# Kernel optimization log

Hardware: AMD Instinct MI355X
Metric: run time of the kernel (lower is better)

## Reference

```python
import jax, jax.numpy as jnp
import numpy as np

N_SRC = 100000
N_DST = 100000
E = 500000
D = 128
L = 2


def _sage(x_src, x_dst, e_src, e_dst, W_self, W_neigh, b):
    # DGL SAGEConv('mean'): out = x_dst @ W_self^T + mean_neighbors(x_src) @ W_neigh^T + b
    n_dst = x_dst.shape[0]
    msg_sum = jax.ops.segment_sum(x_src[e_src], e_dst, num_segments=n_dst)  # [n_dst, D]
    deg = jax.ops.segment_sum(jnp.ones((e_dst.shape[0],), x_src.dtype), e_dst, num_segments=n_dst)
    h_neigh = msg_sum / jnp.maximum(deg, 1.0)[:, None]  # isolated nodes -> 0
    return x_dst @ W_self.T + h_neigh @ W_neigh.T + b


def setup_inputs() -> dict:
    key = jax.random.key(0)
    ks = jax.random.split(key, 10)
    s = 1.0 / np.sqrt(D)
    return {
        "x_src": jax.random.normal(ks[0], (N_SRC, D), jnp.float32),
        "x_dst": jax.random.normal(ks[1], (N_DST, D), jnp.float32),
        "e_src": jax.random.randint(ks[2], (E,), 0, N_SRC, jnp.int32),
        "e_dst": jax.random.randint(ks[3], (E,), 0, N_DST, jnp.int32),
        "W_ship_self": jax.random.normal(ks[4], (L, D, D), jnp.float32) * s,
        "W_ship_neigh": jax.random.normal(ks[5], (L, D, D), jnp.float32) * s,
        "b_ship": jnp.zeros((L, D), jnp.float32),
        "W_rev_self": jax.random.normal(ks[6], (L, D, D), jnp.float32) * s,
        "W_rev_neigh": jax.random.normal(ks[7], (L, D, D), jnp.float32) * s,
        "b_rev": jnp.zeros((L, D), jnp.float32),
    }


def reference(x_src, x_dst, e_src, e_dst, W_ship_self, W_ship_neigh, b_ship,
              W_rev_self, W_rev_neigh, b_rev):
    h_s, h_d = x_src, x_dst
    n_layers = W_ship_self.shape[0]
    for l in range(n_layers):
        # ('source','ship','destination'): messages source -> destination
        new_d = _sage(h_s, h_d, e_src, e_dst, W_ship_self[l], W_ship_neigh[l], b_ship[l])
        # ('destination','rev_ship','source'): messages destination -> source
        new_s = _sage(h_d, h_s, e_dst, e_src, W_rev_self[l], W_rev_neigh[l], b_rev[l])
        h_d = jax.nn.relu(new_d)
        h_s = jax.nn.relu(new_s)
        # dropout p=0.0 (eval) -> identity
    return h_s, h_d
```

## Files before the change

### kernel.cpp

```cpp
#include <hip/hip_runtime.h>
#include <hip/hip_bf16.h>

#define NN 100000
#define EDGES 500000
#define DD 128
#define NBKT 196
#define SLACK 3584
#define CHUNK 4096
#define BPD ((EDGES + CHUNK - 1) / CHUNK)

typedef short bf16x8 __attribute__((ext_vector_type(8)));
typedef float f32x4  __attribute__((ext_vector_type(4)));
typedef float f32x2  __attribute__((ext_vector_type(2)));

__device__ __forceinline__ unsigned short f2bf(float f) {
    unsigned u = __float_as_uint(f);
    u += 0x7fffu + ((u >> 16) & 1u);
    return (unsigned short)(u >> 16);
}

__global__ void f2bx_kernel(const float* __restrict__ a, const float* __restrict__ b,
                            unsigned short* __restrict__ oa, unsigned short* __restrict__ ob) {
    const float* in = blockIdx.y ? b : a;
    unsigned short* out = blockIdx.y ? ob : oa;
    int i = blockIdx.x * 256 + threadIdx.x;
    float4 v = ((const float4*)in)[i];
    ushort4 o;
    o.x = f2bf(v.x); o.y = f2bf(v.y); o.z = f2bf(v.z); o.w = f2bf(v.w);
    ((ushort4*)out)[i] = o;
}

__global__ void f2bw_kernel(const float* __restrict__ w0, const float* __restrict__ w1,
                            const float* __restrict__ w2, const float* __restrict__ w3,
                            unsigned short* __restrict__ o0, unsigned short* __restrict__ o1,
                            unsigned short* __restrict__ o2, unsigned short* __restrict__ o3) {
    const float* in; unsigned short* out;
    switch (blockIdx.y) {
        case 0: in = w0; out = o0; break;
        case 1: in = w1; out = o1; break;
        case 2: in = w2; out = o2; break;
        default: in = w3; out = o3; break;
    }
    int i = blockIdx.x * 256 + threadIdx.x;
    float4 v = ((const float4*)in)[i];
    ushort4 o;
    o.x = f2bf(v.x); o.y = f2bf(v.y); o.z = f2bf(v.z); o.w = f2bf(v.w);
    ((ushort4*)out)[i] = o;
}

__global__ __launch_bounds__(256) void bin_scatter_kernel(
    const int* __restrict__ e_src, const int* __restrict__ e_dst,
    int* __restrict__ gcnt,
    unsigned* __restrict__ recbin)
{
    const int dir = blockIdx.y;
    const int t = threadIdx.x;
    const int c0 = blockIdx.x * CHUNK;
    const int nvalid = min(CHUNK, EDGES - c0);
    const int* __restrict__ TGT = dir ? e_src : e_dst;
    const int* __restrict__ PAY = dir ? e_dst : e_src;

    __shared__ int hist[256];
    __shared__ int lbase[256];
    __shared__ int lofs[256];
    __shared__ int scanA[256], scanB[256];
    __shared__ int laddr[CHUNK];
    __shared__ unsigned lrec[CHUNK];

    hist[t] = 0;
    __syncthreads();

    int myb[16], myslot[16];
    unsigned myrec[16];
    #pragma unroll
    for (int j = 0; j < 16; ++j) {
        int e = c0 + j * 256 + t;
        myb[j] = -1;
        if (e < EDGES) {
            int tgt = TGT[e], pay = PAY[e];
            int b = tgt >> 9;
            myb[j] = b;
            myrec[j] = ((unsigned)pay << 9) | (unsigned)(tgt & 511);
            myslot[j] = atomicAdd(&hist[b], 1);
        }
    }
    __syncthreads();
    int cnt = hist[t];
    lbase[t] = (cnt > 0) ? atomicAdd(&gcnt[dir * 256 + t], cnt) : 0;
    scanA[t] = cnt;
    __syncthreads();
    int* pa = scanA; int* pb = scanB;
    for (int d = 1; d < 256; d <<= 1) {
        pb[t] = pa[t] + (t >= d ? pa[t - d] : 0);
        __syncthreads();
        int* tmp = pa; pa = pb; pb = tmp;
    }
    lofs[t] = pa[t] - cnt;
    __syncthreads();
    #pragma unroll
    for (int j = 0; j < 16; ++j) {
        if (myb[j] >= 0) {
            int b = myb[j];
            int pos = lofs[b] + myslot[j];
            int g = lbase[b] + myslot[j];
            lrec[pos] = myrec[j];
            laddr[pos] = (g < SLACK) ? (b * SLACK + g) : -1;
        }
    }
    __syncthreads();
    unsigned* __restrict__ out = recbin + (size_t)dir * NBKT * SLACK;
    #pragma unroll
    for (int j = 0; j < 16; ++j) {
        int i = j * 256 + t;
        if (i < nvalid) {
            int a = laddr[i];
            if (a >= 0) out[a] = lrec[i];
        }
    }
}

__global__ void bucket_scan_kernel(const int* __restrict__ gcnt, int* __restrict__ csr_base) {
    int t = threadIdx.x;
    __shared__ int A[256], B[256];
    for (int dir = 0; dir < 2; ++dir) {
        int c = (t < NBKT) ? min(gcnt[dir * 256 + t], SLACK) : 0;
        A[t] = c;
        __syncthreads();
        int* pa = A; int* pb = B;
        for (int d = 1; d < 256; d <<= 1) {
            pb[t] = pa[t] + (t >= d ? pa[t - d] : 0);
            __syncthreads();
            int* tmp = pa; pa = pb; pb = tmp;
        }
        if (t < NBKT) csr_base[dir * 200 + t] = pa[t] - c;
        if (t == 0)   csr_base[dir * 200 + NBKT] = pa[255];
        __syncthreads();
    }
}

__global__ __launch_bounds__(256) void fine_place_kernel(
    const unsigned* __restrict__ recbin, const int* __restrict__ gcnt,
    const int* __restrict__ csr_base,
    int* __restrict__ rp_dst, int* __restrict__ rp_src,
    float* __restrict__ inv_dst, float* __restrict__ inv_src,
    int* __restrict__ csr_dst, int* __restrict__ csr_src)
{
    const int dir = blockIdx.y;
    const int bkt = blockIdx.x;
    const int t = threadIdx.x;
    int*   __restrict__ rp  = dir ? rp_src  : rp_dst;
    float* __restrict__ inv = dir ? inv_src : inv_dst;
    int*   __restrict__ csr = dir ? csr_src : csr_dst;
    const unsigned* __restrict__ recs = recbin + ((size_t)dir * NBKT + bkt) * SLACK;
    const int cnt = min(gcnt[dir * 256 + bkt], SLACK);
    const int cbase = csr_base[dir * 200 + bkt];
    const int n0 = bkt * 512;

    __shared__ int deg[512];
    __shared__ int sA[512], sB[512];
    __shared__ int cur[512];
    deg[t] = 0; deg[t + 256] = 0;
    __syncthreads();
    for (int i = t; i < cnt; i += 256)
        atomicAdd(&deg[recs[i] & 511u], 1);
    __syncthreads();
    sA[t] = deg[t]; sA[t + 256] = deg[t + 256];
    __syncthreads();
    int* pa = sA; int* pb = sB;
    for (int d = 1; d < 512; d <<= 1) {
        pb[t]       = pa[t]       + (t >= d           ? pa[t - d]       : 0);
        pb[t + 256] = pa[t + 256] + ((t + 256) >= d   ? pa[t + 256 - d] : 0);
        __syncthreads();
        int* tmp = pa; pa = pb; pb = tmp;
    }
    #pragma unroll
    for (int k = 0; k < 2; ++k) {
        int i = t + k * 256;
        int off = pa[i] - deg[i];
        cur[i] = off;
        int node = n0 + i;
        if (node < NN) {
            rp[node] = cbase + off;
            inv[node] = 1.0f / (float)max(deg[i], 1);
        }
    }
    if (bkt == NBKT - 1 && t == 0) rp[NN] = csr_base[dir * 200 + NBKT];
    __syncthreads();
    for (int i = t; i < cnt; i += 256) {
        unsigned r = recs[i];
        int p = atomicAdd(&cur[r & 511u], 1);
        csr[cbase + p] = (int)(r >> 9);
    }
}

__global__ __launch_bounds__(256) void aggregate3_kernel(
    const unsigned short* __restrict__ h0, const int* __restrict__ rp0,
    const int* __restrict__ csr0, unsigned short* __restrict__ ag0,
    const unsigned short* __restrict__ h1, const int* __restrict__ rp1,
    const int* __restrict__ csr1, unsigned short* __restrict__ ag1)
{
    const int dir = blockIdx.y;
    const unsigned short* __restrict__ h = dir ? h1 : h0;
    const int* __restrict__ rp   = dir ? rp1 : rp0;
    const int* __restrict__ csr  = dir ? csr1 : csr0;
    unsigned short* __restrict__ agg = dir ? ag1 : ag0;

    const int t  = blockIdx.x * 256 + threadIdx.x;
    const int g  = t >> 4;
    const int sl = t & 15;

    const int beg = rp[g], end = rp[g + 1];
    const unsigned short* __restrict__ hp = h + sl * 8;

    f32x2 acc[4];
    #pragma unroll
    for (int k = 0; k < 4; ++k) acc[k] = (f32x2){0.f, 0.f};

    int cidx[8];
    #pragma unroll
    for (int j = 0; j < 8; ++j)
        cidx[j] = (beg + j < end) ? csr[beg + j] : -1;

    bf16x8 v[8];
    #pragma unroll
    for (int j = 0; j < 8; ++j)
        if (cidx[j] >= 0)
            v[j] = *(const bf16x8*)(hp + (size_t)cidx[j] * DD);

    #pragma unroll
    for (int j = 0; j < 8; ++j) {
        if (cidx[j] >= 0) {
            const unsigned* pu = (const unsigned*)&v[j];
            #pragma unroll
            for (int k = 0; k < 4; ++k) {
                unsigned u = pu[k];
                acc[k] += (f32x2){__uint_as_float(u << 16),
                                  __uint_as_float(u & 0xffff0000u)};
            }
        }
    }

    for (int i = beg + 8; i < end; ++i) {
        int c = csr[i];
        bf16x8 w = *(const bf16x8*)(hp + (size_t)c * DD);
        const unsigned* pu = (const unsigned*)&w;
        #pragma unroll
        for (int k = 0; k < 4; ++k) {
            unsigned u = pu[k];
            acc[k] += (f32x2){__uint_as_float(u << 16),
                              __uint_as_float(u & 0xffff0000u)};
        }
    }

    const float sc = 1.0f / (float)max(end - beg, 1);
    uint4 ov;
    ov.x = (unsigned)f2bf(acc[0].x * sc) | ((unsigned)f2bf(acc[0].y * sc) << 16);
    ov.y = (unsigned)f2bf(acc[1].x * sc) | ((unsigned)f2bf(acc[1].y * sc) << 16);
    ov.z = (unsigned)f2bf(acc[2].x * sc) | ((unsigned)f2bf(acc[2].y * sc) << 16);
    ov.w = (unsigned)f2bf(acc[3].x * sc) | ((unsigned)f2bf(acc[3].y * sc) << 16);
    *(uint4*)(agg + (size_t)g * DD + sl * 8) = ov;
}

__global__ __launch_bounds__(512, 4) void mfma_gemm6_kernel(
    const unsigned short* __restrict__ Hs0, const unsigned short* __restrict__ Ha0,
    const unsigned short* __restrict__ Ws0, const unsigned short* __restrict__ Wn0,
    const float* __restrict__ bias0, float* __restrict__ outF0, unsigned short* __restrict__ outB0,
    const unsigned short* __restrict__ Hs1, const unsigned short* __restrict__ Ha1,
    const unsigned short* __restrict__ Ws1, const unsigned short* __restrict__ Wn1,
    const float* __restrict__ bias1, float* __restrict__ outF1, unsigned short* __restrict__ outB1,
    int M)
{
    const int dir = blockIdx.y;
    const unsigned short* __restrict__ Hself = dir ? Hs1 : Hs0;
    const unsigned short* __restrict__ Hagg  = dir ? Ha1 : Ha0;
    const unsigned short* __restrict__ Wself = dir ? Ws1 : Ws0;
    const unsigned short* __restrict__ Wneigh= dir ? Wn1 : Wn0;
    const float* __restrict__ bias = dir ? bias1 : bias0;
    float* __restrict__ outF = dir ? outF1 : outF0;
    unsigned short* __restrict__ outB = dir ? outB1 : outB0;

    __shared__ __align__(16) unsigned short sW[128 * 256];
    const int tid  = threadIdx.x;
    const int lane = tid & 63;
    const int w    = tid >> 6;
    const int row0 = blockIdx.x * 512;

    #pragma unroll
    for (int i = 0; i < 8; ++i) {
        int q = i * 512 + tid;
        int n = q >> 5, c = q & 31;
        const unsigned short* src = (c < 16) ? (Wself + n * 128 + c * 8)
                                             : (Wneigh + n * 128 + (c - 16) * 8);
        int d = n * 256 + (c & 24) * 8 + (((c ^ n) & 7) * 8);
        *(uint4*)(sW + d) = *(const uint4*)src;
    }

    const int mbase = (w >> 1) * 64;
    const int nbase = (w & 1) * 64;
    const int l15 = lane & 15;
    const int l4  = lane >> 4;

    __syncthreads();

    #pragma unroll
    for (int h = 0; h < 2; ++h) {
        const int r0 = row0 + h * 256;

        int voff[4];
        #pragma unroll
        for (int mt = 0; mt < 4; ++mt) {
            int grow = r0 + mbase + mt * 16 + l15;
            if (grow >= M) grow = M - 1;
            voff[mt] = grow * 128 + l4 * 8;
        }

        f32x4 acc[4][4];
        #pragma unroll
        for (int mt = 0; mt < 4; ++mt)
            #pragma unroll
            for (int nt = 0; nt < 4; ++nt) acc[mt][nt] = (f32x4){0.f, 0.f, 0.f, 0.f};

        bf16x8 a_cur[4], a_nxt[4];
        #pragma unroll
        for (int mt = 0; mt < 4; ++mt) a_cur[mt] = *(const bf16x8*)(Hself + voff[mt]);

        #pragma unroll
        for (int ks = 0; ks < 8; ++ks) {
            if (ks < 7) {
                const int ks1 = ks + 1;
                const int col = (ks1 & 3) * 32;
                const unsigned short* __restrict__ base = (ks1 < 4) ? Hself : Hagg;
                #pragma unroll
                for (int mt = 0; mt < 4; ++mt)
                    a_nxt[mt] = *(const bf16x8*)(base + voff[mt] + col);
            }
            const int c = ks * 4 + l4;
            bf16x8 b[4];
            #pragma unroll
            for (int nt = 0; nt < 4; ++nt) {
                int n = nbase + nt * 16 + l15;
                b[nt] = *(const bf16x8*)(sW + n * 256 + (c & 24) * 8 + (((c ^ n) & 7) * 8));
            }
            #pragma unroll
            for (int mt = 0; mt < 4; ++mt) {
                acc[mt][0] = __builtin_amdgcn_mfma_f32_16x16x32_bf16(a_cur[mt], b[0], acc[mt][0], 0, 0, 0);
                acc[mt][1] = __builtin_amdgcn_mfma_f32_16x16x32_bf16(a_cur[mt], b[1], acc[mt][1], 0, 0, 0);
                acc[mt][2] = __builtin_amdgcn_mfma_f32_16x16x32_bf16(a_cur[mt], b[2], acc[mt][2], 0, 0, 0);
                acc[mt][3] = __builtin_amdgcn_mfma_f32_16x16x32_bf16(a_cur[mt], b[3], acc[mt][3], 0, 0, 0);
            }
            #pragma unroll
            for (int mt = 0; mt < 4; ++mt) a_cur[mt] = a_nxt[mt];
        }

        #pragma unroll
        for (int nt = 0; nt < 4; ++nt) {
            int col = nbase + nt * 16 + l15;
            float bj = bias[col];
            #pragma unroll
            for (int mt = 0; mt < 4; ++mt) {
                #pragma unroll
                for (int r = 0; r < 4; ++r) {
                    int grow = r0 + mbase + mt * 16 + l4 * 4 + r;
                    if (grow < M) {
                        float v = fmaxf(acc[mt][nt][r] + bj, 0.f);
                        if (outF) outF[(size_t)grow * 128 + col] = v;
                        else      outB[(size_t)grow * 128 + col] = f2bf(v);
                    }
                }
            }
        }
    }
}

extern "C" void kernel_launch(void* const* d_in, const int* in_sizes, int n_in,
                              void* d_out, int out_size, void* d_ws, size_t ws_size,
                              hipStream_t stream) {
    const float* x_src        = (const float*)d_in[0];
    const float* x_dst        = (const float*)d_in[1];
    const int*   e_src        = (const int*)d_in[2];
    const int*   e_dst        = (const int*)d_in[3];
    const float* W_ship_self  = (const float*)d_in[4];
    const float* W_ship_neigh = (const float*)d_in[5];
    const float* b_ship       = (const float*)d_in[6];
    const float* W_rev_self   = (const float*)d_in[7];
    const float* W_rev_neigh  = (const float*)d_in[8];
    const float* b_rev        = (const float*)d_in[9];
    float* out = (float*)d_out;

    char* ws = (char*)d_ws;
    size_t off = 0;
    auto alloc = [&](size_t bytes) {
        char* p = ws + off;
        off = (off + bytes + 255) & ~(size_t)255;
        return p;
    };
    unsigned short* xs_bf = (unsigned short*)alloc((size_t)NN * DD * 2);
    unsigned short* xd_bf = (unsigned short*)alloc((size_t)NN * DD * 2);
    unsigned short* agg1  = (unsigned short*)alloc((size_t)NN * DD * 2);
    unsigned short* agg2  = (unsigned short*)alloc((size_t)NN * DD * 2);
    unsigned short* Wss_bf = (unsigned short*)alloc(2 * DD * DD * 2);
    unsigned short* Wsn_bf = (unsigned short*)alloc(2 * DD * DD * 2);
    unsigned short* Wrs_bf = (unsigned short*)alloc(2 * DD * DD * 2);
    unsigned short* Wrn_bf = (unsigned short*)alloc(2 * DD * DD * 2);
    int* gcnt = (int*)alloc(2 * 256 * 4);
    int* csr_base = (int*)alloc(2 * 200 * 4);
    unsigned* recbin = (unsigned*)alloc((size_t)2 * NBKT * SLACK * 4);
    int* rp_dst = (int*)alloc((NN + 1) * 4);
    int* rp_src = (int*)alloc((NN + 1) * 4);
    float* inv_dst = (float*)alloc(NN * 4);
    float* inv_src = (float*)alloc(NN * 4);
    int* csr_dst = (int*)alloc(EDGES * 4);
    int* csr_src = (int*)alloc(EDGES * 4);
    (void)ws_size; (void)in_sizes; (void)n_in; (void)out_size;

    hipMemsetAsync(gcnt, 0, 2 * 256 * 4, stream);

    const int xn4 = NN * DD / 4;
    f2bx_kernel<<<dim3(xn4 / 256, 2), 256, 0, stream>>>(x_src, x_dst, xs_bf, xd_bf);
    f2bw_kernel<<<dim3(32, 4), 256, 0, stream>>>(W_ship_self, W_ship_neigh, W_rev_self, W_rev_neigh,
                                                 Wss_bf, Wsn_bf, Wrs_bf, Wrn_bf);

    bin_scatter_kernel<<<dim3(BPD, 2), 256, 0, stream>>>(e_src, e_dst, gcnt, recbin);
    bucket_scan_kernel<<<1, 256, 0, stream>>>(gcnt, csr_base);
    fine_place_kernel<<<dim3(NBKT, 2), 256, 0, stream>>>(recbin, gcnt, csr_base,
        rp_dst, rp_src, inv_dst, inv_src, csr_dst, csr_src);

    float* out_s = out;
    float* out_d = out + (size_t)NN * DD;
    const int gemm_grid = (NN + 511) / 512;
    const int agg_grid  = NN * 16 / 256;

    for (int l = 0; l < 2; ++l) {
        aggregate3_kernel<<<dim3(agg_grid, 2), 256, 0, stream>>>(
            xs_bf, rp_dst, csr_dst, agg1,
            xd_bf, rp_src, csr_src, agg2);
        mfma_gemm6_kernel<<<dim3(gemm_grid, 2), 512, 0, stream>>>(
            xd_bf, agg1, Wss_bf + l * DD * DD, Wsn_bf + l * DD * DD, b_ship + l * DD,
            l ? out_d : nullptr, l ? nullptr : xd_bf,
            xs_bf, agg2, Wrs_bf + l * DD * DD, Wrn_bf + l * DD * DD, b_rev + l * DD,
            l ? out_s : nullptr, l ? nullptr : xs_bf,
            NN);
    }
}
```

Baseline: 427.8 us.

## Split GEMM output columns across blocks and ping-pong layer-one features

The fused self+neighbor GEMM now launches 256-thread blocks covering 256 rows and one 64-column half of the output, with the column half chosen by blockIdx.y. Each block stages only half of the weights in LDS, which means more, smaller blocks for better occupancy and load balance. The cost is that every A row is read twice, once per column half. Because the two column halves of a row are now written by different blocks while the other still reads the old features, layer-0 outputs go to separate ping-pong buffers (xs2/xd2) rather than being written in place.

```diff
diff --git a/kernel.cpp b/kernel.cpp
--- a/kernel.cpp
+++ b/kernel.cpp
@@ -261,7 +261,7 @@
     *(uint4*)(agg + (size_t)g * DD + sl * 8) = ov;
 }
 
-__global__ __launch_bounds__(512, 4) void mfma_gemm6_kernel(
+__global__ __launch_bounds__(256, 4) void mfma_gemm7_kernel(
     const unsigned short* __restrict__ Hs0, const unsigned short* __restrict__ Ha0,
     const unsigned short* __restrict__ Ws0, const unsigned short* __restrict__ Wn0,
     const float* __restrict__ bias0, float* __restrict__ outF0, unsigned short* __restrict__ outB0,
@@ -270,7 +270,8 @@
     const float* __restrict__ bias1, float* __restrict__ outF1, unsigned short* __restrict__ outB1,
     int M)
 {
-    const int dir = blockIdx.y;
+    const int dir = blockIdx.y >> 1;
+    const int nh  = blockIdx.y & 1;
     const unsigned short* __restrict__ Hself = dir ? Hs1 : Hs0;
     const unsigned short* __restrict__ Hagg  = dir ? Ha1 : Ha0;
     const unsigned short* __restrict__ Wself = dir ? Ws1 : Ws0;
@@ -279,93 +280,87 @@
     float* __restrict__ outF = dir ? outF1 : outF0;
     unsigned short* __restrict__ outB = dir ? outB1 : outB0;
 
-    __shared__ __align__(16) unsigned short sW[128 * 256];
+    __shared__ __align__(16) unsigned short sW[64 * 256];
     const int tid  = threadIdx.x;
     const int lane = tid & 63;
     const int w    = tid >> 6;
-    const int row0 = blockIdx.x * 512;
+    const int row0 = blockIdx.x * 256;
 
     #pragma unroll
     for (int i = 0; i < 8; ++i) {
-        int q = i * 512 + tid;
+        int q = i * 256 + tid;
         int n = q >> 5, c = q & 31;
-        const unsigned short* src = (c < 16) ? (Wself + n * 128 + c * 8)
-                                             : (Wneigh + n * 128 + (c - 16) * 8);
+        const unsigned short* src = (c < 16) ? (Wself  + (nh * 64 + n) * 128 + c * 8)
+                                             : (Wneigh + (nh * 64 + n) * 128 + (c - 16) * 8);
         int d = n * 256 + (c & 24) * 8 + (((c ^ n) & 7) * 8);
         *(uint4*)(sW + d) = *(const uint4*)src;
     }
 
-    const int mbase = (w >> 1) * 64;
-    const int nbase = (w & 1) * 64;
+    const int mbase = w * 64;
     const int l15 = lane & 15;
     const int l4  = lane >> 4;
 
-    __syncthreads();
-
-    #pragma unroll
-    for (int h = 0; h < 2; ++h) {
-        const int r0 = row0 + h * 256;
-
-        int voff[4];
+    int voff[4];
+    #pragma unroll
+    for (int mt = 0; mt < 4; ++mt) {
+        int grow = row0 + mbase + mt * 16 + l15;
+        if (grow >= M) grow = M - 1;
+        voff[mt] = grow * 128 + l4 * 8;
+    }
+
+    f32x4 acc[4][4];
+    #pragma unroll
+    for (int mt = 0; mt < 4; ++mt)
+        #pragma unroll
+        for (int nt = 0; nt < 4; ++nt) acc[mt][nt] = (f32x4){0.f, 0.f, 0.f, 0.f};
+
+    __syncthreads();
+
+    bf16x8 a_cur[4], a_nxt[4];
+    #pragma unroll
+    for (int mt = 0; mt < 4; ++mt) a_cur[mt] = *(const bf16x8*)(Hself + voff[mt]);
+
+    #pragma unroll
+    for (int ks = 0; ks < 8; ++ks) {
+        if (ks < 7) {
+            const int ks1 = ks + 1;
+            const int col = (ks1 & 3) * 32;
+            const unsigned short* __restrict__ base = (ks1 < 4) ? Hself : Hagg;
+            #pragma unroll
+            for (int mt = 0; mt < 4; ++mt)
+                a_nxt[mt] = *(const bf16x8*)(base + voff[mt] + col);
+        }
+        const int c = ks * 4 + l4;
+        bf16x8 b[4];
+        #pragma unroll
+        for (int nt = 0; nt < 4; ++nt) {
+            int n = nt * 16 + l15;
+            b[nt] = *(const bf16x8*)(sW + n * 256 + (c & 24) * 8 + (((c ^ n) & 7) * 8));
+        }
         #pragma unroll
         for (int mt = 0; mt < 4; ++mt) {
-            int grow = r0 + mbase + mt * 16 + l15;
-            if (grow >= M) grow = M - 1;
-            voff[mt] = grow * 128 + l4 * 8;
-        }
-
-        f32x4 acc[4][4];
-        #pragma unroll
-        for (int mt = 0; mt < 4; ++mt)
+            acc[mt][0] = __builtin_amdgcn_mfma_f32_16x16x32_bf16(a_cur[mt], b[0], acc[mt][0], 0, 0, 0);
+            acc[mt][1] = __builtin_amdgcn_mfma_f32_16x16x32_bf16(a_cur[mt], b[1], acc[mt][1], 0, 0, 0);
+            acc[mt][2] = __builtin_amdgcn_mfma_f32_16x16x32_bf16(a_cur[mt], b[2], acc[mt][2], 0, 0, 0);
+            acc[mt][3] = __builtin_amdgcn_mfma_f32_16x16x32_bf16(a_cur[mt], b[3], acc[mt][3], 0, 0, 0);
+        }
+        #pragma unroll
+        for (int mt = 0; mt < 4; ++mt) a_cur[mt] = a_nxt[mt];
+    }
+
+    #pragma unroll
+    for (int nt = 0; nt < 4; ++nt) {
+        int col = nh * 64 + nt * 16 + l15;
+        float bj = bias[col];
+        #pragma unroll
+        for (int mt = 0; mt < 4; ++mt) {
             #pragma unroll
-            for (int nt = 0; nt < 4; ++nt) acc[mt][nt] = (f32x4){0.f, 0.f, 0.f, 0.f};
-
-        bf16x8 a_cur[4], a_nxt[4];
-        #pragma unroll
-        for (int mt = 0; mt < 4; ++mt) a_cur[mt] = *(const bf16x8*)(Hself + voff[mt]);
-
-        #pragma unroll
-        for (int ks = 0; ks < 8; ++ks) {
-            if (ks < 7) {
-                const int ks1 = ks + 1;
-                const int col = (ks1 & 3) * 32;
-                const unsigned short* __restrict__ base = (ks1 < 4) ? Hself : Hagg;
-                #pragma unroll
-                for (int mt = 0; mt < 4; ++mt)
-                    a_nxt[mt] = *(const bf16x8*)(base + voff[mt] + col);
-            }
-            const int c = ks * 4 + l4;
-            bf16x8 b[4];
-            #pragma unroll
-            for (int nt = 0; nt < 4; ++nt) {
-                int n = nbase + nt * 16 + l15;
-                b[nt] = *(const bf16x8*)(sW + n * 256 + (c & 24) * 8 + (((c ^ n) & 7) * 8));
-            }
-            #pragma unroll
-            for (int mt = 0; mt < 4; ++mt) {
-                acc[mt][0] = __builtin_amdgcn_mfma_f32_16x16x32_bf16(a_cur[mt], b[0], acc[mt][0], 0, 0, 0);
-                acc[mt][1] = __builtin_amdgcn_mfma_f32_16x16x32_bf16(a_cur[mt], b[1], acc[mt][1], 0, 0, 0);
-                acc[mt][2] = __builtin_amdgcn_mfma_f32_16x16x32_bf16(a_cur[mt], b[2], acc[mt][2], 0, 0, 0);
-                acc[mt][3] = __builtin_amdgcn_mfma_f32_16x16x32_bf16(a_cur[mt], b[3], acc[mt][3], 0, 0, 0);
-            }
-            #pragma unroll
-            for (int mt = 0; mt < 4; ++mt) a_cur[mt] = a_nxt[mt];
-        }
-
-        #pragma unroll
-        for (int nt = 0; nt < 4; ++nt) {
-            int col = nbase + nt * 16 + l15;
-            float bj = bias[col];
-            #pragma unroll
-            for (int mt = 0; mt < 4; ++mt) {
-                #pragma unroll
-                for (int r = 0; r < 4; ++r) {
-                    int grow = r0 + mbase + mt * 16 + l4 * 4 + r;
-                    if (grow < M) {
-                        float v = fmaxf(acc[mt][nt][r] + bj, 0.f);
-                        if (outF) outF[(size_t)grow * 128 + col] = v;
-                        else      outB[(size_t)grow * 128 + col] = f2bf(v);
-                    }
+            for (int r = 0; r < 4; ++r) {
+                int grow = row0 + mbase + mt * 16 + l4 * 4 + r;
+                if (grow < M) {
+                    float v = fmaxf(acc[mt][nt][r] + bj, 0.f);
+                    if (outF) outF[(size_t)grow * 128 + col] = v;
+                    else      outB[(size_t)grow * 128 + col] = f2bf(v);
                 }
             }
         }
@@ -394,10 +389,12 @@
         off = (off + bytes + 255) & ~(size_t)255;
         return p;
     };
-    unsigned short* xs_bf = (unsigned short*)alloc((size_t)NN * DD * 2);
-    unsigned short* xd_bf = (unsigned short*)alloc((size_t)NN * DD * 2);
-    unsigned short* agg1  = (unsigned short*)alloc((size_t)NN * DD * 2);
-    unsigned short* agg2  = (unsigned short*)alloc((size_t)NN * DD * 2);
+    unsigned short* xs_bf  = (unsigned short*)alloc((size_t)NN * DD * 2);
+    unsigned short* xd_bf  = (unsigned short*)alloc((size_t)NN * DD * 2);
+    unsigned short* xs2_bf = (unsigned short*)alloc((size_t)NN * DD * 2);
+    unsigned short* xd2_bf = (unsigned short*)alloc((size_t)NN * DD * 2);
+    unsigned short* agg1   = (unsigned short*)alloc((size_t)NN * DD * 2);
+    unsigned short* agg2   = (unsigned short*)alloc((size_t)NN * DD * 2);
     unsigned short* Wss_bf = (unsigned short*)alloc(2 * DD * DD * 2);
     unsigned short* Wsn_bf = (unsigned short*)alloc(2 * DD * DD * 2);
     unsigned short* Wrs_bf = (unsigned short*)alloc(2 * DD * DD * 2);
@@ -427,18 +424,20 @@
 
     float* out_s = out;
     float* out_d = out + (size_t)NN * DD;
-    const int gemm_grid = (NN + 511) / 512;
+    const int gemm_grid = (NN + 255) / 256;
     const int agg_grid  = NN * 16 / 256;
 
     for (int l = 0; l < 2; ++l) {
+        const unsigned short* hs = l ? xs2_bf : xs_bf;
+        const unsigned short* hd = l ? xd2_bf : xd_bf;
         aggregate3_kernel<<<dim3(agg_grid, 2), 256, 0, stream>>>(
-            xs_bf, rp_dst, csr_dst, agg1,
-            xd_bf, rp_src, csr_src, agg2);
-        mfma_gemm6_kernel<<<dim3(gemm_grid, 2), 512, 0, stream>>>(
-            xd_bf, agg1, Wss_bf + l * DD * DD, Wsn_bf + l * DD * DD, b_ship + l * DD,
-            l ? out_d : nullptr, l ? nullptr : xd_bf,
-            xs_bf, agg2, Wrs_bf + l * DD * DD, Wrn_bf + l * DD * DD, b_rev + l * DD,
-            l ? out_s : nullptr, l ? nullptr : xs_bf,
+            hs, rp_dst, csr_dst, agg1,
+            hd, rp_src, csr_src, agg2);
+        mfma_gemm7_kernel<<<dim3(gemm_grid, 4), 256, 0, stream>>>(
+            hd, agg1, Wss_bf + l * DD * DD, Wsn_bf + l * DD * DD, b_ship + l * DD,
+            l ? out_d : nullptr, l ? nullptr : xd2_bf,
+            hs, agg2, Wrs_bf + l * DD * DD, Wrn_bf + l * DD * DD, b_rev + l * DD,
+            l ? out_s : nullptr, l ? nullptr : xs2_bf,
             NN);
     }
 }
```

New measurement: 449.1 us. 1.05x slower.
